# Kernel optimization log

Hardware: AMD Instinct MI355X
Metric: run time of the kernel (lower is better)

Reference implementation:

```python
import jax, jax.numpy as jnp
import numpy as np

IN_FEATURES = 896
OUT_FEATURES = 151936  # Qwen2.5 vocab
BATCH, SEQ = 2, 1024


def setup_inputs() -> dict:
    key = jax.random.key(0)
    k1, k2, k3 = jax.random.split(key, 3)
    x = jax.random.normal(k1, (BATCH, SEQ, IN_FEATURES), dtype=jnp.float32)
    # int8-range quantized weights stored as int32 (values in [-127, 127])
    quant_weight = jax.random.randint(k2, (OUT_FEATURES, IN_FEATURES), -127, 128, dtype=jnp.int32)
    # per-output-row scales (positive, small)
    scales = jax.random.uniform(k3, (OUT_FEATURES,), dtype=jnp.float32, minval=0.001, maxval=0.02)
    return {"x": x, "quant_weight": quant_weight, "scales": scales}


def reference(x, quant_weight, scales):
    # dequantize: W = int8_weight * per_row_scale  -> [out, in]
    w = quant_weight.astype(x.dtype) * scales.astype(x.dtype)[:, None]
    # F.linear(x, W, None) == x @ W.T : [b, s, in] x [out, in] -> [b, s, out]
    return jnp.einsum('bsi,oi->bso', x, w)
```

## Files before the change

kernel.cpp:

```cpp
#include <hip/hip_runtime.h>
#include <hip/hip_bf16.h>


#define M_DIM 2048
#define N_DIM 151936
#define K_DIM 896

#define BM 128
#define BN 128
#define BK 64
#define NKT (K_DIM / BK)
#define MB_CNT (M_DIM / BM)
#define NB_CNT (N_DIM / BN)
#define NWG (MB_CNT * NB_CNT)

typedef __attribute__((ext_vector_type(8))) short bf16x8;
typedef __attribute__((ext_vector_type(4))) float f32x4;
typedef __attribute__((ext_vector_type(4))) int   i32x4;
typedef __attribute__((ext_vector_type(4))) unsigned int u32x4;
typedef __attribute__((ext_vector_type(2))) unsigned int u32x2;

static __device__ __forceinline__ unsigned short f2bf(float f) {
    unsigned int u = __builtin_bit_cast(unsigned int, f);
    u += 0x7FFFu + ((u >> 16) & 1u);
    return (unsigned short)(u >> 16);
}
static __device__ __forceinline__ unsigned int pack2(float lo, float hi) {
    return (unsigned int)f2bf(lo) | ((unsigned int)f2bf(hi) << 16);
}
static __device__ __forceinline__ void gload_lds16(const void* g, void* l) {
    __builtin_amdgcn_global_load_lds(
        (const __attribute__((address_space(1))) unsigned int*)g,
        (__attribute__((address_space(3))) unsigned int*)l, 16, 0, 0);
}


__global__ void quant_x_kernel(const float* __restrict__ X,
                               signed char* __restrict__ Xq,
                               float* __restrict__ Sx) {
    const int row  = blockIdx.x * 4 + (threadIdx.x >> 6);
    const int lane = threadIdx.x & 63;
    const float* xr = X + (size_t)row * K_DIM;
    float v[14];
    float am = 0.f;
    #pragma unroll
    for (int i = 0; i < 14; ++i) {
        v[i] = xr[lane + i * 64];
        am = fmaxf(am, fabsf(v[i]));
    }
    #pragma unroll
    for (int off = 32; off > 0; off >>= 1)
        am = fmaxf(am, __shfl_xor(am, off));
    am = fmaxf(am, 1e-20f);
    const float inv = 127.f / am;
    if (lane == 0) Sx[row] = am / 127.f;
    signed char* qr = Xq + (size_t)row * K_DIM;
    #pragma unroll
    for (int i = 0; i < 14; ++i)
        qr[lane + i * 64] = (signed char)(int)rintf(v[i] * inv);
}

__global__ void cvt_w8_kernel(const int* __restrict__ Wq,
                              signed char* __restrict__ W8) {
    const long n8 = (long)N_DIM * K_DIM / 8;
    for (long i = (long)blockIdx.x * blockDim.x + threadIdx.x; i < n8;
         i += (long)gridDim.x * blockDim.x) {
        i32x4 a = ((const i32x4*)Wq)[2 * i];
        i32x4 b = ((const i32x4*)Wq)[2 * i + 1];
        unsigned int lo = (unsigned int)(a[0] & 0xff) |
                          ((unsigned int)(a[1] & 0xff) << 8) |
                          ((unsigned int)(a[2] & 0xff) << 16) |
                          ((unsigned int)(a[3] & 0xff) << 24);
        unsigned int hi = (unsigned int)(b[0] & 0xff) |
                          ((unsigned int)(b[1] & 0xff) << 8) |
                          ((unsigned int)(b[2] & 0xff) << 16) |
                          ((unsigned int)(b[3] & 0xff) << 24);
        u32x2 o; o[0] = lo; o[1] = hi;
        ((u32x2*)W8)[i] = o;
    }
}


#define SCHED0 __builtin_amdgcn_sched_barrier(0)
#define VMCNT(N) asm volatile("s_waitcnt vmcnt(" #N ")" ::: "memory")
#define LGKM0    asm volatile("s_waitcnt lgkmcnt(0)" ::: "memory")

__global__ __launch_bounds__(256, 3)
void lmhead_gemm_i8(const signed char* __restrict__ Xq,
                    const signed char* __restrict__ W8,
                    const float* __restrict__ Sw,
                    const float* __restrict__ Sx,
                    float* __restrict__ O)
{
    __shared__ signed char lds[3][2][BM][BK];

    const int tid  = threadIdx.x;
    const int lane = tid & 63;
    const int wave = tid >> 6;
    const int wr   = wave >> 1;
    const int wc   = wave & 1;

    const int bid = blockIdx.x;
    const int wg  = (bid & 7) * (NWG / 8) + (bid >> 3);
    const int mb  = wg % MB_CNT;
    const int nb  = wg / MB_CNT;

    const int lslot = (lane & 3) ^ ((lane >> 3) & 3);
    const signed char* srcA0 =
        Xq + (size_t)(mb * BM + wave * 16 + (lane >> 2)) * K_DIM + lslot * 16;
    const signed char* srcA1 = srcA0 + (size_t)64 * K_DIM;
    const signed char* srcB0 =
        W8 + (size_t)(nb * BN + wave * 16 + (lane >> 2)) * K_DIM + lslot * 16;
    const signed char* srcB1 = srcB0 + (size_t)64 * K_DIM;

    auto stage = [&](int b3, int k0) {
        gload_lds16(srcA0 + k0, &lds[b3][0][wave * 16][0]);
        gload_lds16(srcA1 + k0, &lds[b3][0][64 + wave * 16][0]);
        gload_lds16(srcB0 + k0, &lds[b3][1][wave * 16][0]);
        gload_lds16(srcB1 + k0, &lds[b3][1][64 + wave * 16][0]);
    };

    const int physoff   = ((lane >> 4) ^ ((lane >> 1) & 3)) * 16;
    const int arow_base = wr * 64 + (lane & 15);
    const int brow_base = wc * 64 + (lane & 15);

    i32x4 acc[4][4];
    #pragma unroll
    for (int i = 0; i < 4; ++i)
        #pragma unroll
        for (int j = 0; j < 4; ++j)
            acc[i][j] = i32x4{0, 0, 0, 0};

    stage(0, 0);
    stage(1, BK);
    SCHED0;
    VMCNT(4);
    SCHED0;
    __builtin_amdgcn_s_barrier();
    SCHED0;

    i32x4 af[4], bfr[4];

#define READ_AB(B3) do { \
    _Pragma("unroll") \
    for (int mf = 0; mf < 4; ++mf) \
        af[mf] = *(const i32x4*)&lds[B3][0][arow_base + mf * 16][physoff]; \
    _Pragma("unroll") \
    for (int nf = 0; nf < 4; ++nf) \
        bfr[nf] = *(const i32x4*)&lds[B3][1][brow_base + nf * 16][physoff]; \
} while (0)
#define MFMA16() do { \
    __builtin_amdgcn_s_setprio(1); \
    _Pragma("unroll") \
    for (int mf = 0; mf < 4; ++mf) { \
        _Pragma("unroll") \
        for (int nf = 0; nf < 4; ++nf) \
            acc[mf][nf] = __builtin_amdgcn_mfma_i32_16x16x64_i8( \
                af[mf], bfr[nf], acc[mf][nf], 0, 0, 0); \
    } \
    __builtin_amdgcn_s_setprio(0); \
} while (0)

    for (int t = 0; t < NKT - 2; ++t) {
        const int cur = t % 3;
        READ_AB(cur);
        stage((t + 2) % 3, (t + 2) * BK);
        SCHED0;
        VMCNT(4);
        LGKM0;
        SCHED0;
        __builtin_amdgcn_s_barrier();
        SCHED0;
        MFMA16();
    }

    {
        READ_AB((NKT - 2) % 3);
        SCHED0;
        VMCNT(0);
        LGKM0;
        SCHED0;
        __builtin_amdgcn_s_barrier();
        SCHED0;
        MFMA16();
    }
    {
        READ_AB((NKT - 1) % 3);
        SCHED0;
        LGKM0;
        SCHED0;
        MFMA16();
    }

#undef READ_AB
#undef MFMA16

    __syncthreads();

    float* lf = (float*)&lds[0][0][0][0];
    const int qw = lane >> 4;
    const int li = lane & 15;

    float scn[4];
    #pragma unroll
    for (int nf = 0; nf < 4; ++nf)
        scn[nf] = Sw[nb * BN + wc * 64 + nf * 16 + li];

    #pragma unroll
    for (int p = 0; p < 2; ++p) {
        if (p) __syncthreads();
        if (wr == p) {
            #pragma unroll
            for (int a = 0; a < 4; ++a) {
                #pragma unroll
                for (int nf = 0; nf < 4; ++nf) {
                    #pragma unroll
                    for (int r = 0; r < 4; ++r) {
                        const int lr   = a * 16 + qw * 4 + r;
                        const int col  = wc * 64 + nf * 16 + li;
                        const int pcol = col ^ (qw << 4);
                        lf[lr * 128 + pcol] = (float)acc[a][nf][r] * scn[nf];
                    }
                }
            }
        }
        __syncthreads();
        #pragma unroll
        for (int i = 0; i < 8; ++i) {
            const int row = wave * 16 + i * 2 + (lane >> 5);
            const int q   = (row >> 2) & 3;
            const int pch = (lane & 31) ^ (q << 2);
            f32x4 v = *(const f32x4*)&lf[row * 128 + pch * 4];
            const size_t grow = (size_t)(mb * BM + p * 64 + row);
            const float sxr = Sx[grow];
            v *= sxr;
            const size_t gcol = (size_t)(nb * BN + (lane & 31) * 4);
            *(f32x4*)&O[grow * N_DIM + gcol] = v;
        }
    }
}


#define FBM 128
#define FBN 128
#define FBK 32
#define FNSTEPS (K_DIM / FBK)
#define FMB (M_DIM / FBM)
#define FNB (N_DIM / FBN)
#define FNWG (FMB * FNB)

__global__ __launch_bounds__(256, 2)
void lmhead_gemm_conv(const float* __restrict__ X,
                      const int* __restrict__ Wq,
                      const float* __restrict__ S,
                      float* __restrict__ O)
{
    __shared__ unsigned short Alds[2][FBM][FBK];
    __shared__ unsigned short Blds2[2][FBN][FBK];

    const int tid  = threadIdx.x;
    const int lane = tid & 63;
    const int wave = tid >> 6;
    const int wr   = wave >> 1;
    const int wc   = wave & 1;

    const int bid = blockIdx.x;
    const int wg  = (bid & 7) * (FNWG / 8) + (bid >> 3);
    const int mb  = wg % FMB;
    const int nb  = wg / FMB;

    const int srow = tid >> 1;
    const int skh  = (tid & 1) * 16;

    const float* aptr = X  + (size_t)(mb * FBM + srow) * K_DIM + skh;
    const int*   wptr = Wq + (size_t)(nb * FBN + srow) * K_DIM + skh;

    f32x4 av[4];
    i32x4 wv[4];

    auto load_tiles = [&](int k0) {
        const f32x4* ap = (const f32x4*)(aptr + k0);
        const i32x4* wp = (const i32x4*)(wptr + k0);
        av[0] = ap[0]; av[1] = ap[1]; av[2] = ap[2]; av[3] = ap[3];
        wv[0] = wp[0]; wv[1] = wp[1]; wv[2] = wp[2]; wv[3] = wp[3];
    };

    auto stage = [&](int buf) {
        unsigned int apk[8], wpk[8];
        #pragma unroll
        for (int i = 0; i < 8; ++i) {
            apk[i] = pack2(av[(2*i) >> 2][(2*i) & 3], av[(2*i+1) >> 2][(2*i+1) & 3]);
            wpk[i] = pack2((float)wv[(2*i) >> 2][(2*i) & 3], (float)wv[(2*i+1) >> 2][(2*i+1) & 3]);
        }
        *(u32x4*)&Alds[buf][srow][skh]      = u32x4{apk[0], apk[1], apk[2], apk[3]};
        *(u32x4*)&Alds[buf][srow][skh + 8]  = u32x4{apk[4], apk[5], apk[6], apk[7]};
        *(u32x4*)&Blds2[buf][srow][skh]     = u32x4{wpk[0], wpk[1], wpk[2], wpk[3]};
        *(u32x4*)&Blds2[buf][srow][skh + 8] = u32x4{wpk[4], wpk[5], wpk[6], wpk[7]};
    };

    f32x4 acc[4][4];
    #pragma unroll
    for (int i = 0; i < 4; ++i)
        #pragma unroll
        for (int j = 0; j < 4; ++j)
            acc[i][j] = f32x4{0.f, 0.f, 0.f, 0.f};

    load_tiles(0);
    stage(0);
    __syncthreads();

    int cur = 0;
    for (int s = 0; s < FNSTEPS; ++s) {
        if (s + 1 < FNSTEPS) load_tiles((s + 1) * FBK);

        bf16x8 af[4], bfr[4];
        const int arow = wr * 64 + (lane & 15);
        const int brow = wc * 64 + (lane & 15);
        const int kb   = (lane >> 4) * 8;
        #pragma unroll
        for (int mf = 0; mf < 4; ++mf)
            af[mf] = *(const bf16x8*)&Alds[cur][arow + mf * 16][kb];
        #pragma unroll
        for (int nf = 0; nf < 4; ++nf)
            bfr[nf] = *(const bf16x8*)&Blds2[cur][brow + nf * 16][kb];

        #pragma unroll
        for (int mf = 0; mf < 4; ++mf)
            #pragma unroll
            for (int nf = 0; nf < 4; ++nf)
                acc[mf][nf] = __builtin_amdgcn_mfma_f32_16x16x32_bf16(
                    af[mf], bfr[nf], acc[mf][nf], 0, 0, 0);

        if (s + 1 < FNSTEPS) stage(cur ^ 1);
        __syncthreads();
        cur ^= 1;
    }

    #pragma unroll
    for (int nf = 0; nf < 4; ++nf) {
        const int n = nb * FBN + wc * 64 + nf * 16 + (lane & 15);
        const float sc = S[n];
        #pragma unroll
        for (int mf = 0; mf < 4; ++mf) {
            const int m0 = mb * FBM + wr * 64 + mf * 16 + ((lane >> 4) << 2);
            #pragma unroll
            for (int r = 0; r < 4; ++r)
                O[(size_t)(m0 + r) * N_DIM + n] = acc[mf][nf][r] * sc;
        }
    }
}


extern "C" void kernel_launch(void* const* d_in, const int* in_sizes, int n_in,
                              void* d_out, int out_size, void* d_ws, size_t ws_size,
                              hipStream_t stream) {
    const float* X  = (const float*)d_in[0];
    const int*   Wq = (const int*)d_in[1];
    const float* S  = (const float*)d_in[2];
    float*       O  = (float*)d_out;

    const size_t XQ_BYTES = (size_t)M_DIM * K_DIM;
    const size_t SX_BYTES = (size_t)M_DIM * sizeof(float);
    const size_t W8_BYTES = (size_t)N_DIM * K_DIM;

    if (ws_size >= XQ_BYTES + SX_BYTES + W8_BYTES) {
        signed char* xq = (signed char*)d_ws;
        float*       sx = (float*)((char*)d_ws + XQ_BYTES);
        signed char* w8 = (signed char*)((char*)d_ws + XQ_BYTES + SX_BYTES);
        quant_x_kernel<<<M_DIM / 4, 256, 0, stream>>>(X, xq, sx);
        cvt_w8_kernel<<<2048, 256, 0, stream>>>(Wq, w8);
        lmhead_gemm_i8<<<NWG, 256, 0, stream>>>(xq, w8, S, sx, O);
    } else {
        lmhead_gemm_conv<<<FNWG, 256, 0, stream>>>(X, Wq, S, O);
    }
}
```

Measured before the change: 701.2 us.

## Double-buffer MFMA fragments in registers to overlap LDS reads with compute

```diff
diff --git a/kernel.cpp b/kernel.cpp
--- a/kernel.cpp
+++ b/kernel.cpp
@@ -131,69 +131,79 @@
         for (int j = 0; j < 4; ++j)
             acc[i][j] = i32x4{0, 0, 0, 0};
 
-    stage(0, 0);
-    stage(1, BK);
-    SCHED0;
-    VMCNT(4);
-    SCHED0;
-    __builtin_amdgcn_s_barrier();
-    SCHED0;
-
-    i32x4 af[4], bfr[4];
-
-#define READ_AB(B3) do { \
+    i32x4 afE[4], bfE[4], afO[4], bfO[4];
+
+#define READ_FRAGS(B3, AF, BF) do { \
     _Pragma("unroll") \
     for (int mf = 0; mf < 4; ++mf) \
-        af[mf] = *(const i32x4*)&lds[B3][0][arow_base + mf * 16][physoff]; \
+        AF[mf] = *(const i32x4*)&lds[B3][0][arow_base + mf * 16][physoff]; \
     _Pragma("unroll") \
     for (int nf = 0; nf < 4; ++nf) \
-        bfr[nf] = *(const i32x4*)&lds[B3][1][brow_base + nf * 16][physoff]; \
+        BF[nf] = *(const i32x4*)&lds[B3][1][brow_base + nf * 16][physoff]; \
 } while (0)
-#define MFMA16() do { \
+#define MFMA16(AF, BF) do { \
     __builtin_amdgcn_s_setprio(1); \
     _Pragma("unroll") \
     for (int mf = 0; mf < 4; ++mf) { \
         _Pragma("unroll") \
         for (int nf = 0; nf < 4; ++nf) \
             acc[mf][nf] = __builtin_amdgcn_mfma_i32_16x16x64_i8( \
-                af[mf], bfr[nf], acc[mf][nf], 0, 0, 0); \
+                AF[mf], BF[nf], acc[mf][nf], 0, 0, 0); \
     } \
     __builtin_amdgcn_s_setprio(0); \
 } while (0)
-
-    for (int t = 0; t < NKT - 2; ++t) {
-        const int cur = t % 3;
-        READ_AB(cur);
-        stage((t + 2) % 3, (t + 2) * BK);
-        SCHED0;
-        VMCNT(4);
-        LGKM0;
-        SCHED0;
+#define BODYF(T, AC, BC, AN, BN_) do { \
+    SCHED0; VMCNT(4); LGKM0; SCHED0; \
+    __builtin_amdgcn_s_barrier(); \
+    SCHED0; \
+    READ_FRAGS(((T) + 1) % 3, AN, BN_); \
+    stage(((T) + 3) % 3, ((T) + 3) * BK); \
+    MFMA16(AC, BC); \
+} while (0)
+#define BODYN(T, AC, BC, AN, BN_) do { \
+    SCHED0; VMCNT(4); LGKM0; SCHED0; \
+    __builtin_amdgcn_s_barrier(); \
+    SCHED0; \
+    READ_FRAGS(((T) + 1) % 3, AN, BN_); \
+    MFMA16(AC, BC); \
+} while (0)
+
+    stage(0, 0);
+    stage(1, BK);
+    SCHED0; VMCNT(4); SCHED0;
+    __builtin_amdgcn_s_barrier();
+    SCHED0;
+    READ_FRAGS(0, afE, bfE);
+    stage(2, 2 * BK);
+
+    BODYF(0,  afE, bfE, afO, bfO);
+    BODYF(1,  afO, bfO, afE, bfE);
+    BODYF(2,  afE, bfE, afO, bfO);
+    BODYF(3,  afO, bfO, afE, bfE);
+    BODYF(4,  afE, bfE, afO, bfO);
+    BODYF(5,  afO, bfO, afE, bfE);
+    BODYF(6,  afE, bfE, afO, bfO);
+    BODYF(7,  afO, bfO, afE, bfE);
+    BODYF(8,  afE, bfE, afO, bfO);
+    BODYF(9,  afO, bfO, afE, bfE);
+    BODYF(10, afE, bfE, afO, bfO);
+    BODYN(11, afO, bfO, afE, bfE);
+    {
+        SCHED0; VMCNT(0); LGKM0; SCHED0;
         __builtin_amdgcn_s_barrier();
         SCHED0;
-        MFMA16();
-    }
-
+        READ_FRAGS(13 % 3, afO, bfO);
+        MFMA16(afE, bfE);
+    }
     {
-        READ_AB((NKT - 2) % 3);
-        SCHED0;
-        VMCNT(0);
-        LGKM0;
-        SCHED0;
-        __builtin_amdgcn_s_barrier();
-        SCHED0;
-        MFMA16();
-    }
-    {
-        READ_AB((NKT - 1) % 3);
-        SCHED0;
-        LGKM0;
-        SCHED0;
-        MFMA16();
-    }
-
-#undef READ_AB
+        SCHED0; LGKM0; SCHED0;
+        MFMA16(afO, bfO);
+    }
+
+#undef READ_FRAGS
 #undef MFMA16
+#undef BODYF
+#undef BODYN
 
     __syncthreads();
 
```

After: 700.7 us. About the same (-0.1%).

## Shrink int8 GEMM tile to 128x64 with double-buffered LDS and higher occupancy

Applied to the files above, without the earlier changes.

```diff
diff --git a/kernel.cpp b/kernel.cpp
--- a/kernel.cpp
+++ b/kernel.cpp
@@ -7,7 +7,7 @@
 #define K_DIM 896
 
 #define BM 128
-#define BN 128
+#define BN 64
 #define BK 64
 #define NKT (K_DIM / BK)
 #define MB_CNT (M_DIM / BM)
@@ -82,17 +82,18 @@
 
 
 #define SCHED0 __builtin_amdgcn_sched_barrier(0)
-#define VMCNT(N) asm volatile("s_waitcnt vmcnt(" #N ")" ::: "memory")
-#define LGKM0    asm volatile("s_waitcnt lgkmcnt(0)" ::: "memory")
-
-__global__ __launch_bounds__(256, 3)
+#define VMCNT0 asm volatile("s_waitcnt vmcnt(0)" ::: "memory")
+#define LGKM0  asm volatile("s_waitcnt lgkmcnt(0)" ::: "memory")
+
+__global__ __launch_bounds__(256, 5)
 void lmhead_gemm_i8(const signed char* __restrict__ Xq,
                     const signed char* __restrict__ W8,
                     const float* __restrict__ Sw,
                     const float* __restrict__ Sx,
                     float* __restrict__ O)
 {
-    __shared__ signed char lds[3][2][BM][BK];
+    __shared__ signed char ldsA[2][BM][BK];
+    __shared__ signed char ldsB[2][BN][BK];
 
     const int tid  = threadIdx.x;
     const int lane = tid & 63;
@@ -106,105 +107,84 @@
     const int nb  = wg / MB_CNT;
 
     const int lslot = (lane & 3) ^ ((lane >> 3) & 3);
-    const signed char* srcA0 =
-        Xq + (size_t)(mb * BM + wave * 16 + (lane >> 2)) * K_DIM + lslot * 16;
-    const signed char* srcA1 = srcA0 + (size_t)64 * K_DIM;
-    const signed char* srcB0 =
+    const signed char* srcA =
+        Xq + (size_t)(mb * BM + wave * 32 + (lane >> 2)) * K_DIM + lslot * 16;
+    const signed char* srcB =
         W8 + (size_t)(nb * BN + wave * 16 + (lane >> 2)) * K_DIM + lslot * 16;
-    const signed char* srcB1 = srcB0 + (size_t)64 * K_DIM;
-
-    auto stage = [&](int b3, int k0) {
-        gload_lds16(srcA0 + k0, &lds[b3][0][wave * 16][0]);
-        gload_lds16(srcA1 + k0, &lds[b3][0][64 + wave * 16][0]);
-        gload_lds16(srcB0 + k0, &lds[b3][1][wave * 16][0]);
-        gload_lds16(srcB1 + k0, &lds[b3][1][64 + wave * 16][0]);
+
+    auto stage = [&](int b2, int k0) {
+        gload_lds16(srcA + k0, &ldsA[b2][wave * 32][0]);
+        gload_lds16(srcA + (size_t)16 * K_DIM + k0, &ldsA[b2][wave * 32 + 16][0]);
+        gload_lds16(srcB + k0, &ldsB[b2][wave * 16][0]);
     };
 
     const int physoff   = ((lane >> 4) ^ ((lane >> 1) & 3)) * 16;
     const int arow_base = wr * 64 + (lane & 15);
-    const int brow_base = wc * 64 + (lane & 15);
-
-    i32x4 acc[4][4];
+    const int brow_base = wc * 32 + (lane & 15);
+
+    i32x4 acc[4][2];
     #pragma unroll
     for (int i = 0; i < 4; ++i)
         #pragma unroll
-        for (int j = 0; j < 4; ++j)
+        for (int j = 0; j < 2; ++j)
             acc[i][j] = i32x4{0, 0, 0, 0};
 
     stage(0, 0);
-    stage(1, BK);
     SCHED0;
-    VMCNT(4);
+    VMCNT0;
     SCHED0;
     __builtin_amdgcn_s_barrier();
     SCHED0;
 
-    i32x4 af[4], bfr[4];
-
-#define READ_AB(B3) do { \
+    i32x4 af[4], bfr[2];
+
+#define READ_AB(B2) do { \
     _Pragma("unroll") \
     for (int mf = 0; mf < 4; ++mf) \
-        af[mf] = *(const i32x4*)&lds[B3][0][arow_base + mf * 16][physoff]; \
+        af[mf] = *(const i32x4*)&ldsA[B2][arow_base + mf * 16][physoff]; \
     _Pragma("unroll") \
-    for (int nf = 0; nf < 4; ++nf) \
-        bfr[nf] = *(const i32x4*)&lds[B3][1][brow_base + nf * 16][physoff]; \
+    for (int nf = 0; nf < 2; ++nf) \
+        bfr[nf] = *(const i32x4*)&ldsB[B2][brow_base + nf * 16][physoff]; \
 } while (0)
-#define MFMA16() do { \
+#define MFMA8() do { \
     __builtin_amdgcn_s_setprio(1); \
     _Pragma("unroll") \
     for (int mf = 0; mf < 4; ++mf) { \
         _Pragma("unroll") \
-        for (int nf = 0; nf < 4; ++nf) \
+        for (int nf = 0; nf < 2; ++nf) \
             acc[mf][nf] = __builtin_amdgcn_mfma_i32_16x16x64_i8( \
                 af[mf], bfr[nf], acc[mf][nf], 0, 0, 0); \
     } \
     __builtin_amdgcn_s_setprio(0); \
 } while (0)
 
-    for (int t = 0; t < NKT - 2; ++t) {
-        const int cur = t % 3;
+    #pragma unroll 2
+    for (int t = 0; t < NKT; ++t) {
+        const int cur = t & 1;
         READ_AB(cur);
-        stage((t + 2) % 3, (t + 2) * BK);
+        if (t < NKT - 1) stage(cur ^ 1, (t + 1) * BK);
         SCHED0;
-        VMCNT(4);
+        VMCNT0;
         LGKM0;
         SCHED0;
         __builtin_amdgcn_s_barrier();
         SCHED0;
-        MFMA16();
-    }
-
-    {
-        READ_AB((NKT - 2) % 3);
-        SCHED0;
-        VMCNT(0);
-        LGKM0;
-        SCHED0;
-        __builtin_amdgcn_s_barrier();
-        SCHED0;
-        MFMA16();
-    }
-    {
-        READ_AB((NKT - 1) % 3);
-        SCHED0;
-        LGKM0;
-        SCHED0;
-        MFMA16();
+        MFMA8();
     }
 
 #undef READ_AB
-#undef MFMA16
+#undef MFMA8
 
     __syncthreads();
 
-    float* lf = (float*)&lds[0][0][0][0];
+    float* lf = (float*)&ldsA[0][0][0];
     const int qw = lane >> 4;
     const int li = lane & 15;
 
-    float scn[4];
-    #pragma unroll
-    for (int nf = 0; nf < 4; ++nf)
-        scn[nf] = Sw[nb * BN + wc * 64 + nf * 16 + li];
+    float scn[2];
+    #pragma unroll
+    for (int nf = 0; nf < 2; ++nf)
+        scn[nf] = Sw[nb * BN + wc * 32 + nf * 16 + li];
 
     #pragma unroll
     for (int p = 0; p < 2; ++p) {
@@ -213,28 +193,28 @@
             #pragma unroll
             for (int a = 0; a < 4; ++a) {
                 #pragma unroll
-                for (int nf = 0; nf < 4; ++nf) {
+                for (int nf = 0; nf < 2; ++nf) {
                     #pragma unroll
                     for (int r = 0; r < 4; ++r) {
                         const int lr   = a * 16 + qw * 4 + r;
-                        const int col  = wc * 64 + nf * 16 + li;
+                        const int col  = wc * 32 + nf * 16 + li;
                         const int pcol = col ^ (qw << 4);
-                        lf[lr * 128 + pcol] = (float)acc[a][nf][r] * scn[nf];
+                        lf[lr * 64 + pcol] = (float)acc[a][nf][r] * scn[nf];
                     }
                 }
             }
         }
         __syncthreads();
         #pragma unroll
-        for (int i = 0; i < 8; ++i) {
-            const int row = wave * 16 + i * 2 + (lane >> 5);
-            const int q   = (row >> 2) & 3;
-            const int pch = (lane & 31) ^ (q << 2);
-            f32x4 v = *(const f32x4*)&lf[row * 128 + pch * 4];
+        for (int i = 0; i < 4; ++i) {
+            const int row    = i * 16 + (tid >> 4);
+            const int lane16 = tid & 15;
+            const int q      = (row >> 2) & 3;
+            const int pch    = lane16 ^ (q << 2);
+            f32x4 v = *(const f32x4*)&lf[row * 64 + pch * 4];
             const size_t grow = (size_t)(mb * BM + p * 64 + row);
-            const float sxr = Sx[grow];
-            v *= sxr;
-            const size_t gcol = (size_t)(nb * BN + (lane & 31) * 4);
+            v *= Sx[grow];
+            const size_t gcol = (size_t)(nb * BN + lane16 * 4);
             *(f32x4*)&O[grow * N_DIM + gcol] = v;
         }
     }
```

After: 774.3 us. 10.4% more time.
